# Performance work log

Measured on AMD Instinct MI355X. Metric: run time of the kernel, lower is better.

## Reference

```python
import jax, jax.numpy as jnp
import numpy as np

L = 4        # initial_layers (layers actually run in forward)
DIM = 128    # model dim
NB = 8       # num_blocks per layer
K = 2        # max_active blocks per layer
B = 131072   # batch
FIN = 32     # input features (nn.Linear(32, dim))
PRIORITY = 0.5  # fresh block: success_rate*0.6 + excitement*0.4 = 0.5


def setup_inputs() -> dict:
    key = jax.random.key(0)
    ks = jax.random.split(key, 10)
    s = 0.02
    return {
        "x": jax.random.normal(ks[0], (B, FIN), dtype=jnp.float32),
        "proj_w": jax.random.normal(ks[1], (FIN, DIM)) * s,
        "proj_b": jnp.zeros((DIM,)),
        "pos": jax.random.normal(ks[2], (1, 16, DIM)) * 0.02,
        "sel_w": jax.random.normal(ks[3], (L, DIM, NB)) * s,   # per-layer selector
        "sel_b": jnp.zeros((L, NB)),
        "ln_s": jnp.ones((L, NB, DIM)),                         # per-block LayerNorm
        "ln_b": jnp.zeros((L, NB, DIM)),
        "w1": jax.random.normal(ks[4], (L, NB, DIM, 2 * DIM)) * s,
        "b1": jnp.zeros((L, NB, 2 * DIM)),
        "w2": jax.random.normal(ks[5], (L, NB, 2 * DIM, DIM)) * s,
        "b2": jnp.zeros((L, NB, DIM)),
        "gate": jax.random.normal(ks[6], (L, NB, DIM)) * 0.01,  # torsion_gate
        "cls_w": jax.random.normal(ks[7], (DIM, 2)) * s,
        "cls_b": jnp.zeros((2,)),
        "torsion_field": jnp.zeros((1, DIM)),                   # registered buffer (zeros)
    }


def _block(h, ln_s, ln_b, w1, b1, w2, b2, gate, tf):
    # h: [B, 1, DIM]. LayerNorm(eps=1e-5) -> Linear -> GELU -> Linear -> torsion gate -> 0.5 residual
    mu = h.mean(axis=-1, keepdims=True)
    var = ((h - mu) ** 2).mean(axis=-1, keepdims=True)
    hn = (h - mu) / jnp.sqrt(var + 1e-5) * ln_s + ln_b
    z = jax.nn.gelu(hn @ w1 + b1, approximate=False) @ w2 + b2
    te = jax.nn.sigmoid(gate) * tf           # [1, DIM]
    z = z * (1.0 + te[:, None, :])           # broadcast over seq dim (unsqueeze(1))
    return h + 0.5 * z


def reference(x, proj_w, proj_b, pos, sel_w, sel_b, ln_s, ln_b,
              w1, b1, w2, b2, gate, cls_w, cls_b, torsion_field):
    # input projection + positional slice; seq_len == 1
    h = (x @ proj_w + proj_b)[:, None, :] + pos[:, :1, :]   # [B, 1, DIM]
    for l in range(L):
        scores = jax.nn.sigmoid(h.mean(axis=1) @ sel_w[l] + sel_b[l])  # [B, NB]
        # adjusted[0, i] = scores[0, i]*0.6 + priority*0.4 ; top-k taken on row 0
        adj = scores[0] * 0.6 + PRIORITY * 0.4
        _, top = jax.lax.top_k(adj, K)
        for k in range(K):
            i = top[k]
            h = _block(h, ln_s[l][i], ln_b[l][i], w1[l][i], b1[l][i],
                       w2[l][i], b2[l][i], gate[l][i], torsion_field)
    logits = h.mean(axis=1) @ cls_w + cls_b   # [B, 2]
    return logits, h
```

## Files before the change

### kernel.cpp

```cpp
#include <hip/hip_runtime.h>


typedef __attribute__((ext_vector_type(8))) short s16x8;
typedef __attribute__((ext_vector_type(4))) float f32x4;
typedef __attribute__((ext_vector_type(2))) unsigned u32x2;
typedef unsigned short ushort_t;

#define BATCH 131072
#define TBROWS 32
#define HSTR 132
#define FGSTR 544
#define FQSTR 136

#define WS_IDX 0
#define WS_PRM 64
#define WS_PB  12352
#define WS_PW  12864
#define WS_W1  21056
#define WS_W2  545344
#define WS_DMP 1069632

__device__ inline ushort_t f2bf(float f) {
  unsigned u = __float_as_uint(f);
  u += 0x7fffu + ((u >> 16) & 1u);
  return (ushort_t)(u >> 16);
}
__device__ inline ushort_t f2bf1(float f) {
  return (ushort_t)((__float_as_uint(f) + 0x8000u) >> 16);
}
__device__ inline unsigned f2bf2(float lo, float hi) {
  unsigned a = __float_as_uint(lo) + 0x8000u;
  unsigned b = __float_as_uint(hi) + 0x8000u;
  return __builtin_amdgcn_perm(b, a, 0x07060302u);
}

__device__ inline float dpp_xor1(float v) {
  return __int_as_float(__builtin_amdgcn_update_dpp(
      0, __float_as_int(v), 0xB1 , 0xF, 0xF, true));
}
__device__ inline float dpp_xor2(float v) {
  return __int_as_float(__builtin_amdgcn_update_dpp(
      0, __float_as_int(v), 0x4E , 0xF, 0xF, true));
}

__device__ inline float geluf(float v) {
  float e = __builtin_amdgcn_exp2f(-2.4554670f * v);
  return v * __builtin_amdgcn_rcpf(1.0f + e);
}

__global__ __launch_bounds__(256) void uv6_warm(
    const float* __restrict__ w1, const float* __restrict__ w2,
    float* __restrict__ dump) {
  int gid = blockIdx.x * 256 + threadIdx.x;
  const float4* a = (const float4*)w1;
  const float4* b = (const float4*)w2;
  float s = 0.0f;
#pragma unroll
  for (int i = 0; i < 2; ++i) {
    float4 v = a[gid + i * 131072];
    float4 u = b[gid + i * 131072];
    s += v.x + v.y + v.z + v.w + u.x + u.y + u.z + u.w;
  }
  if (s > 1e30f) dump[0] = s;
}

__global__ __launch_bounds__(1024) void uv6_select(
    const float* __restrict__ x, const float* __restrict__ proj_w,
    const float* __restrict__ proj_b, const float* __restrict__ pos,
    const float* __restrict__ sel_w, const float* __restrict__ sel_b,
    const float* __restrict__ ln_s, const float* __restrict__ ln_b,
    const float* __restrict__ w1, const float* __restrict__ b1,
    const float* __restrict__ w2, const float* __restrict__ b2,
    const float* __restrict__ gate, const float* __restrict__ tf,
    int* __restrict__ wsI) {
  __shared__ float h0[128], hn[128], z1[256];
  __shared__ float red[1024];
  __shared__ float wred[128];
  __shared__ float adjs[8];
  __shared__ int top[2];
  __shared__ float stat[2];
  const int t = threadIdx.x;
  const int lane = t & 63, wv = t >> 6;
  const int n1 = t & 255, dp1 = t >> 8;
  const int n2 = t & 127, dp2 = t >> 7;

  if (t < 128) {
    float a = proj_b[t] + pos[t];
#pragma unroll
    for (int f = 0; f < 32; ++f) a += x[f] * proj_w[f * 128 + t];
    h0[t] = a;
  }
  __syncthreads();

  for (int l = 0; l < 4; ++l) {
    {
      float pp = h0[t >> 3] * sel_w[(l * 128 + (t >> 3)) * 8 + (t & 7)];
      pp += __shfl_xor(pp, 8);
      pp += __shfl_xor(pp, 16);
      pp += __shfl_xor(pp, 32);
      if (lane < 8) wred[wv * 8 + lane] = pp;
    }
    __syncthreads();
    if (t < 8) {
      float sc = sel_b[l * 8 + t];
#pragma unroll
      for (int v = 0; v < 16; ++v) sc += wred[v * 8 + t];
      sc = 1.0f / (1.0f + __expf(-sc));
      adjs[t] = sc * 0.6f + 0.2f;
    }
    __syncthreads();
    if (t == 0) {
      int i0 = 0; float v0 = adjs[0];
      for (int j = 1; j < 8; ++j) if (adjs[j] > v0) { v0 = adjs[j]; i0 = j; }
      int i1 = -1; float v1 = -1e30f;
      for (int j = 0; j < 8; ++j) if (j != i0 && adjs[j] > v1) { v1 = adjs[j]; i1 = j; }
      top[0] = i0; top[1] = i1;
      wsI[2 * l] = i0; wsI[2 * l + 1] = i1;
    }
    __syncthreads();
    for (int kk = 0; kk < 2; ++kk) {
      const int base = l * 8 + top[kk];
      float w1v[32], w2v[32];
      const float* w1p = w1 + (base * 128 + dp1 * 32) * 256 + n1;
      const float* w2p = w2 + (base * 256 + dp2 * 32) * 128 + n2;
#pragma unroll
      for (int j = 0; j < 32; ++j) w1v[j] = w1p[j * 256];
#pragma unroll
      for (int j = 0; j < 32; ++j) w2v[j] = w2p[j * 128];
      if (t < 64) {
        float a = h0[t], b = h0[t + 64];
        float s2 = a + b, q2 = a * a + b * b;
        s2 += __shfl_xor(s2, 1);  q2 += __shfl_xor(q2, 1);
        s2 += __shfl_xor(s2, 2);  q2 += __shfl_xor(q2, 2);
        s2 += __shfl_xor(s2, 4);  q2 += __shfl_xor(q2, 4);
        s2 += __shfl_xor(s2, 8);  q2 += __shfl_xor(q2, 8);
        s2 += __shfl_xor(s2, 16); q2 += __shfl_xor(q2, 16);
        s2 += __shfl_xor(s2, 32); q2 += __shfl_xor(q2, 32);
        if (t == 0) {
          float mu = s2 * (1.0f / 128.0f);
          stat[0] = mu;
          stat[1] = rsqrtf(q2 * (1.0f / 128.0f) - mu * mu + 1e-5f);
        }
      }
      __syncthreads();
      if (t < 128)
        hn[t] = (h0[t] - stat[0]) * stat[1] * ln_s[base * 128 + t] + ln_b[base * 128 + t];
      __syncthreads();
      {
        float a = 0.0f;
#pragma unroll
        for (int j = 0; j < 32; ++j) a += hn[dp1 * 32 + j] * w1v[j];
        red[dp1 * 256 + n1] = a;
      }
      __syncthreads();
      if (t < 256) {
        float z = red[t] + red[256 + t] + red[512 + t] + red[768 + t] + b1[base * 256 + t];
        z1[t] = z * 0.5f * (1.0f + erff(z * 0.70710678118f));
      }
      __syncthreads();
      {
        float a = 0.0f;
#pragma unroll
        for (int j = 0; j < 32; ++j) a += z1[dp2 * 32 + j] * w2v[j];
        red[dp2 * 128 + n2] = a;
      }
      __syncthreads();
      if (t < 128) {
        float z2 = b2[base * 128 + t];
#pragma unroll
        for (int v = 0; v < 8; ++v) z2 += red[v * 128 + t];
        float te = tf[t] * (1.0f / (1.0f + __expf(-gate[base * 128 + t])));
        h0[t] += 0.5f * z2 * (1.0f + te);
      }
      __syncthreads();
    }
  }
}

__global__ __launch_bounds__(256) void uv6_pack(
    const float* __restrict__ w1, const float* __restrict__ w2,
    const float* __restrict__ ln_s, const float* __restrict__ ln_b,
    const float* __restrict__ b1, const float* __restrict__ b2,
    const float* __restrict__ gate, const float* __restrict__ tf,
    const float* __restrict__ proj_w, const float* __restrict__ proj_b,
    const float* __restrict__ pos, const int* __restrict__ wsI,
    ushort_t* __restrict__ w1P, ushort_t* __restrict__ w2P,
    float* __restrict__ wsP, ushort_t* __restrict__ pwP,
    float* __restrict__ pb) {
  const int bx = blockIdx.x;
  const int t = threadIdx.x;
  if (bx < 16) {
    __shared__ ushort_t tile[32768];
    int s = bx >> 1;
    int base = (s >> 1) * 8 + wsI[s];
    if ((bx & 1) == 0) {
      const float* W = w1 + base * 32768;
      const float* LS = ln_s + base * 128;
      int kk = t >> 6, n4 = (t & 63) * 4;
#pragma unroll
      for (int it = 0; it < 16; ++it) {
        int k = it * 8 + kk * 2;
        float4 v0 = *(const float4*)(W + k * 256 + n4);
        float4 v1 = *(const float4*)(W + (k + 1) * 256 + n4);
        float s0 = LS[k], s1 = LS[k + 1];
        int pk = (k >> 5) * 512 + ((k >> 3) & 3) * 128 + (k & 7);
        const float* e0 = (const float*)&v0;
        const float* e1 = (const float*)&v1;
#pragma unroll
        for (int i = 0; i < 4; ++i) {
          int n = n4 + i;
          int pos_ = (n >> 4) * 2048 + pk + (n & 15) * 8;
          *(unsigned*)&tile[pos_] =
              (unsigned)f2bf(e0[i] * s0) | ((unsigned)f2bf(e1[i] * s1) << 16);
        }
      }
      __syncthreads();
      ushort_t* dst = w1P + s * 32768;
#pragma unroll
      for (int it = 0; it < 16; ++it)
        *(uint4*)(dst + (it * 256 + t) * 8) = *(const uint4*)(tile + (it * 256 + t) * 8);
    } else {
      const float* W = w2 + base * 32768;
      int kk = t >> 5, n4 = (t & 31) * 4;
      float te4[4];
#pragma unroll
      for (int i = 0; i < 4; ++i)
        te4[i] = 0.5f * (1.0f + tf[n4 + i] *
                 (1.0f / (1.0f + __expf(-gate[base * 128 + n4 + i]))));
#pragma unroll
      for (int it = 0; it < 16; ++it) {
        int k = it * 16 + kk * 2;
        float4 v0 = *(const float4*)(W + k * 128 + n4);
        float4 v1 = *(const float4*)(W + (k + 1) * 128 + n4);
        int pk = (k >> 5) * 512 + ((k >> 3) & 3) * 128 + (k & 7);
        const float* e0 = (const float*)&v0;
        const float* e1 = (const float*)&v1;
#pragma unroll
        for (int i = 0; i < 4; ++i) {
          int n = n4 + i;
          int pos_ = (n >> 4) * 4096 + pk + (n & 15) * 8;
          *(unsigned*)&tile[pos_] =
              (unsigned)f2bf(e0[i] * te4[i]) | ((unsigned)f2bf(e1[i] * te4[i]) << 16);
        }
      }
      __syncthreads();
      ushort_t* dst = w2P + s * 32768;
#pragma unroll
      for (int it = 0; it < 16; ++it)
        *(uint4*)(dst + (it * 256 + t) * 8) = *(const uint4*)(tile + (it * 256 + t) * 8);
    }
    return;
  }
  if (bx < 24) {
    int s = bx - 16, n = t;
    int base = (s >> 1) * 8 + wsI[s];
    float a = b1[base * 256 + n];
#pragma unroll 16
    for (int k = 0; k < 128; ++k)
      a += ln_b[base * 128 + k] * w1[(base * 128 + k) * 256 + n];
    wsP[s * 384 + n] = a;
    if (n < 128) {
      float te = tf[n] * (1.0f / (1.0f + __expf(-gate[base * 128 + n])));
      wsP[s * 384 + 256 + n] = 0.5f * (1.0f + te) * b2[base * 128 + n];
    }
    return;
  }
  int gid = (bx - 24) * 256 + t;
  if (gid < 4096) {
    int j = gid & 7, ln = (gid >> 3) & 63, nt = gid >> 9;
    int k = (ln >> 4) * 8 + j, n = nt * 16 + (ln & 15);
    pwP[gid] = f2bf(proj_w[k * 128 + n]);
  } else if (gid < 4224) {
    int d = gid - 4096;
    pb[d] = proj_b[d] + pos[d];
  }
}

__global__ __launch_bounds__(256, 4) void uv6_main(
    const float* __restrict__ x, const float* __restrict__ cls_w,
    const float* __restrict__ cls_b, const float* __restrict__ wsP,
    const float* __restrict__ pb, const ushort_t* __restrict__ pwP,
    const ushort_t* __restrict__ w1P, const ushort_t* __restrict__ w2P,
    float* __restrict__ out) {
  __shared__ float hbuf[TBROWS * HSTR];
  __shared__ ushort_t frag[16 * FGSTR];

  const int tid = threadIdx.x;
  const int w = tid >> 6, lane = tid & 63, q = lane >> 4, m0 = lane & 15;
  const int r = tid >> 3, p = tid & 7;
  const int rt_r = r >> 4, m_r = r & 15;
  const long rowbase = (long)blockIdx.x * TBROWS;
  ushort_t* fb = &frag[q * FQSTR + m0 * 8];

  {
    float4 xv = *(const float4*)(x + (rowbase + r) * 32 + p * 4);
    unsigned u01 = f2bf2(xv.x, xv.y), u23 = f2bf2(xv.z, xv.w);
    ushort_t* dst = &frag[(rt_r * 8) * FGSTR + (p >> 1) * FQSTR + m_r * 8 + (p & 1) * 4];
    *(unsigned*)dst = u01;
    *(unsigned*)(dst + 2) = u23;
  }
  __syncthreads();

  {
    s16x8 bp0 = *(const s16x8*)(pwP + ((2 * w + 0) * 64 + lane) * 8);
    s16x8 bp1 = *(const s16x8*)(pwP + ((2 * w + 1) * 64 + lane) * 8);
    float bv0 = pb[(2 * w + 0) * 16 + m0];
    float bv1 = pb[(2 * w + 1) * 16 + m0];
    f32x4 acc[2][2];
#pragma unroll
    for (int rt = 0; rt < 2; ++rt) {
      acc[rt][0] = (f32x4){bv0, bv0, bv0, bv0};
      acc[rt][1] = (f32x4){bv1, bv1, bv1, bv1};
    }
#pragma unroll
    for (int rt = 0; rt < 2; ++rt) {
      s16x8 af = *(const s16x8*)&fb[(rt * 8) * FGSTR];
      acc[rt][0] = __builtin_amdgcn_mfma_f32_16x16x32_bf16(af, bp0, acc[rt][0], 0, 0, 0);
      acc[rt][1] = __builtin_amdgcn_mfma_f32_16x16x32_bf16(af, bp1, acc[rt][1], 0, 0, 0);
    }
#pragma unroll
    for (int rt = 0; rt < 2; ++rt)
#pragma unroll
      for (int ni = 0; ni < 2; ++ni) {
        int col = (2 * w + ni) * 16 + m0;
#pragma unroll
        for (int reg = 0; reg < 4; ++reg)
          hbuf[(rt * 16 + 4 * q + reg) * HSTR + col] = acc[rt][ni][reg];
      }
  }
  __syncthreads();

  float* outH = out + (size_t)BATCH * 2;

  for (int s = 0; s < 8; ++s) {
    const float* c1 = wsP + s * 384;
    const float* c2 = c1 + 256;
    const ushort_t* w1s = w1P + s * 32768;
    const ushort_t* w2s = w2P + s * 32768;

    s16x8 bfr1[4][4];
#pragma unroll
    for (int ni = 0; ni < 4; ++ni)
#pragma unroll
      for (int ks = 0; ks < 4; ++ks)
        bfr1[ni][ks] = *(const s16x8*)(w1s + (((4 * w + ni) * 4 + ks) * 64 + lane) * 8);

    {
      const float* hr = hbuf + r * HSTR + p * 16;
      float hv[16];
#pragma unroll
      for (int i = 0; i < 4; ++i)
        *(float4*)(hv + i * 4) = *(const float4*)(hr + i * 4);
      float sum = 0.0f, ssq = 0.0f;
#pragma unroll
      for (int i = 0; i < 16; ++i) { sum += hv[i]; ssq += hv[i] * hv[i]; }
      sum += dpp_xor1(sum); ssq += dpp_xor1(ssq);
      sum += dpp_xor2(sum); ssq += dpp_xor2(ssq);
      sum += __shfl_xor(sum, 4); ssq += __shfl_xor(ssq, 4);
      float mu = sum * (1.0f / 128.0f);
      float rstd = rsqrtf(ssq * (1.0f / 128.0f) - mu * mu + 1e-5f);
      float nmu = -mu * rstd;
#pragma unroll
      for (int g = 0; g < 2; ++g) {
        union { unsigned u[4]; s16x8 v; } tv;
#pragma unroll
        for (int jj = 0; jj < 4; ++jj) {
          float a = fmaf(hv[g * 8 + jj * 2], rstd, nmu);
          float b = fmaf(hv[g * 8 + jj * 2 + 1], rstd, nmu);
          tv.u[jj] = f2bf2(a, b);
        }
        int kb = p >> 1, kq = (p & 1) * 2 + g;
        *(s16x8*)&frag[(rt_r * 8 + kb) * FGSTR + kq * FQSTR + m_r * 8] = tv.v;
      }
    }
    __syncthreads();

    f32x4 a1[2][4];
#pragma unroll
    for (int ni = 0; ni < 4; ++ni) {
      f32x4 bv = *(const f32x4*)&c1[(4 * w + ni) * 16 + 4 * q];
#pragma unroll
      for (int rt = 0; rt < 2; ++rt) a1[rt][ni] = bv;
    }
#pragma unroll
    for (int ks = 0; ks < 4; ++ks) {
      s16x8 hf[2];
#pragma unroll
      for (int rt = 0; rt < 2; ++rt)
        hf[rt] = *(const s16x8*)&fb[(rt * 8 + ks) * FGSTR];
#pragma unroll
      for (int rt = 0; rt < 2; ++rt)
#pragma unroll
        for (int ni = 0; ni < 4; ++ni)
          a1[rt][ni] = __builtin_amdgcn_mfma_f32_16x16x32_bf16(bfr1[ni][ks], hf[rt], a1[rt][ni], 0, 0, 0);
    }
    __syncthreads();

    s16x8 bfr2[2][8];
#pragma unroll
    for (int ni = 0; ni < 2; ++ni)
#pragma unroll
      for (int ks = 0; ks < 8; ++ks)
        bfr2[ni][ks] = *(const s16x8*)(w2s + (((2 * w + ni) * 8 + ks) * 64 + lane) * 8);
    float cv0 = c2[(2 * w + 0) * 16 + m0];
    float cv1 = c2[(2 * w + 1) * 16 + m0];

    {
      int j0 = 4 * (q & 1), kqb = q >> 1;
#pragma unroll
      for (int ni = 0; ni < 4; ++ni) {
        int kb = 2 * w + (ni >> 1);
        int kq = (2 * ni + kqb) & 3;
#pragma unroll
        for (int rt = 0; rt < 2; ++rt) {
          unsigned lo = f2bf2(geluf(a1[rt][ni][0]), geluf(a1[rt][ni][1]));
          unsigned hi = f2bf2(geluf(a1[rt][ni][2]), geluf(a1[rt][ni][3]));
          *(u32x2*)&frag[(rt * 8 + kb) * FGSTR + kq * FQSTR + m0 * 8 + j0] =
              (u32x2){lo, hi};
        }
      }
    }
    __syncthreads();

    f32x4 a2[2][2];
#pragma unroll
    for (int rt = 0; rt < 2; ++rt) {
      a2[rt][0] = (f32x4){cv0, cv0, cv0, cv0};
      a2[rt][1] = (f32x4){cv1, cv1, cv1, cv1};
    }
#pragma unroll
    for (int kb = 0; kb < 8; ++kb) {
      s16x8 af[2];
#pragma unroll
      for (int rt = 0; rt < 2; ++rt)
        af[rt] = *(const s16x8*)&fb[(rt * 8 + kb) * FGSTR];
#pragma unroll
      for (int rt = 0; rt < 2; ++rt) {
        a2[rt][0] = __builtin_amdgcn_mfma_f32_16x16x32_bf16(af[rt], bfr2[0][kb], a2[rt][0], 0, 0, 0);
        a2[rt][1] = __builtin_amdgcn_mfma_f32_16x16x32_bf16(af[rt], bfr2[1][kb], a2[rt][1], 0, 0, 0);
      }
    }

#pragma unroll
    for (int rt = 0; rt < 2; ++rt)
#pragma unroll
      for (int ni = 0; ni < 2; ++ni) {
        int col = (2 * w + ni) * 16 + m0;
#pragma unroll
        for (int reg = 0; reg < 4; ++reg)
          hbuf[(rt * 16 + 4 * q + reg) * HSTR + col] += a2[rt][ni][reg];
      }
    __syncthreads();
  }

#pragma unroll
  for (int it = 0; it < 4; ++it) {
    int p4 = it * 256 + tid;
    int row = p4 >> 5, c = (p4 & 31) * 4;
    float4 o = *(const float4*)(hbuf + row * HSTR + c);
    *(float4*)(outH + rowbase * 128 + p4 * 4) = o;
  }

  {
    const float* hr = hbuf + r * HSTR + p * 16;
    float l0 = 0.0f, l1 = 0.0f;
#pragma unroll
    for (int i = 0; i < 16; i += 4) {
      float4 v = *(const float4*)(hr + i);
      int c = (p * 16 + i) * 2;
      l0 += v.x * cls_w[c] + v.y * cls_w[c + 2] + v.z * cls_w[c + 4] + v.w * cls_w[c + 6];
      l1 += v.x * cls_w[c + 1] + v.y * cls_w[c + 3] + v.z * cls_w[c + 5] + v.w * cls_w[c + 7];
    }
    l0 += dpp_xor1(l0); l1 += dpp_xor1(l1);
    l0 += dpp_xor2(l0); l1 += dpp_xor2(l1);
    l0 += __shfl_xor(l0, 4); l1 += __shfl_xor(l1, 4);
    if (p == 0) {
      float2 lg = {l0 + cls_b[0], l1 + cls_b[1]};
      *(float2*)(out + (rowbase + r) * 2) = lg;
    }
  }
}

extern "C" void kernel_launch(void* const* d_in, const int* in_sizes, int n_in,
                              void* d_out, int out_size, void* d_ws, size_t ws_size,
                              hipStream_t stream) {
  (void)in_sizes; (void)n_in; (void)out_size; (void)ws_size;
  const float* x      = (const float*)d_in[0];
  const float* proj_w = (const float*)d_in[1];
  const float* proj_b = (const float*)d_in[2];
  const float* pos    = (const float*)d_in[3];
  const float* sel_w  = (const float*)d_in[4];
  const float* sel_b  = (const float*)d_in[5];
  const float* ln_s   = (const float*)d_in[6];
  const float* ln_b   = (const float*)d_in[7];
  const float* w1     = (const float*)d_in[8];
  const float* b1     = (const float*)d_in[9];
  const float* w2     = (const float*)d_in[10];
  const float* b2     = (const float*)d_in[11];
  const float* gate   = (const float*)d_in[12];
  const float* cls_w  = (const float*)d_in[13];
  const float* cls_b  = (const float*)d_in[14];
  const float* tf     = (const float*)d_in[15];

  char* ws = (char*)d_ws;
  int* wsI        = (int*)(ws + WS_IDX);
  float* wsP      = (float*)(ws + WS_PRM);
  float* pb       = (float*)(ws + WS_PB);
  ushort_t* pwP   = (ushort_t*)(ws + WS_PW);
  ushort_t* w1P   = (ushort_t*)(ws + WS_W1);
  ushort_t* w2P   = (ushort_t*)(ws + WS_W2);
  float* dump     = (float*)(ws + WS_DMP);
  float* outF     = (float*)d_out;

  uv6_warm<<<512, 256, 0, stream>>>(w1, w2, dump);
  uv6_select<<<1, 1024, 0, stream>>>(x, proj_w, proj_b, pos, sel_w, sel_b, ln_s,
                                     ln_b, w1, b1, w2, b2, gate, tf, wsI);
  uv6_pack<<<41, 256, 0, stream>>>(w1, w2, ln_s, ln_b, b1, b2, gate, tf,
                                   proj_w, proj_b, pos, wsI, w1P, w2P, wsP,
                                   pwP, pb);
  uv6_main<<<BATCH / TBROWS, 256, 0, stream>>>(x, cls_w, cls_b, wsP, pb, pwP,
                                               w1P, w2P, outF);
}
```

Baseline: 362.8 us.

## Rewrite select kernel as single-wave shuffle version; lighter barriers and MFMA priority

The single-block routing kernel moves from 1024 threads with many LDS reductions and __syncthreads to a single 64-lane wave. That wave keeps h in registers and uses shuffles for all reductions and matvecs, which removes barrier latency on this serial critical path but leaves much less parallelism for the weight streaming. The main kernel swaps __syncthreads for an lgkmcnt wait plus raw s_barrier with a sched_barrier, and raises wave priority around the MFMA loops. An unused helper is removed.

```diff
diff --git a/kernel.cpp b/kernel.cpp
--- a/kernel.cpp
+++ b/kernel.cpp
@@ -20,13 +20,16 @@
 #define WS_W2  545344
 #define WS_DMP 1069632
 
+#define BARRIER_LDS() do {                                   \
+    asm volatile("s_waitcnt lgkmcnt(0)" ::: "memory");       \
+    __builtin_amdgcn_s_barrier();                            \
+    __builtin_amdgcn_sched_barrier(0);                       \
+  } while (0)
+
 __device__ inline ushort_t f2bf(float f) {
   unsigned u = __float_as_uint(f);
   u += 0x7fffu + ((u >> 16) & 1u);
   return (ushort_t)(u >> 16);
-}
-__device__ inline ushort_t f2bf1(float f) {
-  return (ushort_t)((__float_as_uint(f) + 0x8000u) >> 16);
 }
 __device__ inline unsigned f2bf2(float lo, float hi) {
   unsigned a = __float_as_uint(lo) + 0x8000u;
@@ -64,7 +67,7 @@
   if (s > 1e30f) dump[0] = s;
 }
 
-__global__ __launch_bounds__(1024) void uv6_select(
+__global__ __launch_bounds__(64) void uv6_select(
     const float* __restrict__ x, const float* __restrict__ proj_w,
     const float* __restrict__ proj_b, const float* __restrict__ pos,
     const float* __restrict__ sel_w, const float* __restrict__ sel_b,
@@ -73,106 +76,102 @@
     const float* __restrict__ w2, const float* __restrict__ b2,
     const float* __restrict__ gate, const float* __restrict__ tf,
     int* __restrict__ wsI) {
-  __shared__ float h0[128], hn[128], z1[256];
-  __shared__ float red[1024];
-  __shared__ float wred[128];
-  __shared__ float adjs[8];
-  __shared__ int top[2];
-  __shared__ float stat[2];
-  const int t = threadIdx.x;
-  const int lane = t & 63, wv = t >> 6;
-  const int n1 = t & 255, dp1 = t >> 8;
-  const int n2 = t & 127, dp2 = t >> 7;
-
-  if (t < 128) {
-    float a = proj_b[t] + pos[t];
-#pragma unroll
-    for (int f = 0; f < 32; ++f) a += x[f] * proj_w[f * 128 + t];
-    h0[t] = a;
-  }
-  __syncthreads();
+  const int lane = threadIdx.x;
+
+  float xv = x[lane & 31];
+  float ha = proj_b[lane] + pos[lane];
+  float hb = proj_b[lane + 64] + pos[lane + 64];
+#pragma unroll
+  for (int f = 0; f < 32; ++f) {
+    float xf = __shfl(xv, f);
+    ha = fmaf(xf, proj_w[f * 128 + lane], ha);
+    hb = fmaf(xf, proj_w[f * 128 + lane + 64], hb);
+  }
 
   for (int l = 0; l < 4; ++l) {
-    {
-      float pp = h0[t >> 3] * sel_w[(l * 128 + (t >> 3)) * 8 + (t & 7)];
-      pp += __shfl_xor(pp, 8);
-      pp += __shfl_xor(pp, 16);
-      pp += __shfl_xor(pp, 32);
-      if (lane < 8) wred[wv * 8 + lane] = pp;
-    }
-    __syncthreads();
-    if (t < 8) {
-      float sc = sel_b[l * 8 + t];
-#pragma unroll
-      for (int v = 0; v < 16; ++v) sc += wred[v * 8 + t];
-      sc = 1.0f / (1.0f + __expf(-sc));
-      adjs[t] = sc * 0.6f + 0.2f;
-    }
-    __syncthreads();
-    if (t == 0) {
-      int i0 = 0; float v0 = adjs[0];
-      for (int j = 1; j < 8; ++j) if (adjs[j] > v0) { v0 = adjs[j]; i0 = j; }
-      int i1 = -1; float v1 = -1e30f;
-      for (int j = 0; j < 8; ++j) if (j != i0 && adjs[j] > v1) { v1 = adjs[j]; i1 = j; }
-      top[0] = i0; top[1] = i1;
-      wsI[2 * l] = i0; wsI[2 * l + 1] = i1;
-    }
-    __syncthreads();
+    float sc[8];
+#pragma unroll
+    for (int n = 0; n < 8; ++n) {
+      sc[n] = fmaf(ha, sel_w[(l * 128 + lane) * 8 + n],
+                   hb * sel_w[(l * 128 + lane + 64) * 8 + n]);
+    }
+#pragma unroll
+    for (int n = 0; n < 8; ++n) {
+      sc[n] += __shfl_xor(sc[n], 1);
+      sc[n] += __shfl_xor(sc[n], 2);
+      sc[n] += __shfl_xor(sc[n], 4);
+      sc[n] += __shfl_xor(sc[n], 8);
+      sc[n] += __shfl_xor(sc[n], 16);
+      sc[n] += __shfl_xor(sc[n], 32);
+    }
+    float adj[8];
+#pragma unroll
+    for (int n = 0; n < 8; ++n) {
+      float s = 1.0f / (1.0f + __expf(-(sc[n] + sel_b[l * 8 + n])));
+      adj[n] = s * 0.6f + 0.2f;
+    }
+    int i0 = 0; float v0 = adj[0];
+#pragma unroll
+    for (int j = 1; j < 8; ++j) if (adj[j] > v0) { v0 = adj[j]; i0 = j; }
+    int i1 = -1; float v1 = -1e30f;
+#pragma unroll
+    for (int j = 0; j < 8; ++j) if (j != i0 && adj[j] > v1) { v1 = adj[j]; i1 = j; }
+    if (lane == 0) { wsI[2 * l] = i0; wsI[2 * l + 1] = i1; }
+
+#pragma unroll 1
     for (int kk = 0; kk < 2; ++kk) {
-      const int base = l * 8 + top[kk];
-      float w1v[32], w2v[32];
-      const float* w1p = w1 + (base * 128 + dp1 * 32) * 256 + n1;
-      const float* w2p = w2 + (base * 256 + dp2 * 32) * 128 + n2;
-#pragma unroll
-      for (int j = 0; j < 32; ++j) w1v[j] = w1p[j * 256];
-#pragma unroll
-      for (int j = 0; j < 32; ++j) w2v[j] = w2p[j * 128];
-      if (t < 64) {
-        float a = h0[t], b = h0[t + 64];
-        float s2 = a + b, q2 = a * a + b * b;
-        s2 += __shfl_xor(s2, 1);  q2 += __shfl_xor(q2, 1);
-        s2 += __shfl_xor(s2, 2);  q2 += __shfl_xor(q2, 2);
-        s2 += __shfl_xor(s2, 4);  q2 += __shfl_xor(q2, 4);
-        s2 += __shfl_xor(s2, 8);  q2 += __shfl_xor(q2, 8);
-        s2 += __shfl_xor(s2, 16); q2 += __shfl_xor(q2, 16);
-        s2 += __shfl_xor(s2, 32); q2 += __shfl_xor(q2, 32);
-        if (t == 0) {
-          float mu = s2 * (1.0f / 128.0f);
-          stat[0] = mu;
-          stat[1] = rsqrtf(q2 * (1.0f / 128.0f) - mu * mu + 1e-5f);
+      const int base = l * 8 + (kk == 0 ? i0 : i1);
+      float s2 = ha + hb, q2 = ha * ha + hb * hb;
+      s2 += __shfl_xor(s2, 1);  q2 += __shfl_xor(q2, 1);
+      s2 += __shfl_xor(s2, 2);  q2 += __shfl_xor(q2, 2);
+      s2 += __shfl_xor(s2, 4);  q2 += __shfl_xor(q2, 4);
+      s2 += __shfl_xor(s2, 8);  q2 += __shfl_xor(q2, 8);
+      s2 += __shfl_xor(s2, 16); q2 += __shfl_xor(q2, 16);
+      s2 += __shfl_xor(s2, 32); q2 += __shfl_xor(q2, 32);
+      float mu = s2 * (1.0f / 128.0f);
+      float rstd = rsqrtf(q2 * (1.0f / 128.0f) - mu * mu + 1e-5f);
+      float na = (ha - mu) * rstd * ln_s[base * 128 + lane] + ln_b[base * 128 + lane];
+      float nb = (hb - mu) * rstd * ln_s[base * 128 + lane + 64] + ln_b[base * 128 + lane + 64];
+
+      float z[4];
+#pragma unroll
+      for (int jj = 0; jj < 4; ++jj) z[jj] = b1[base * 256 + 64 * jj + lane];
+      const float* W1 = w1 + base * 32768;
+#pragma unroll 8
+      for (int d = 0; d < 64; ++d) {
+        float u = __shfl(na, d);
+#pragma unroll
+        for (int jj = 0; jj < 4; ++jj)
+          z[jj] = fmaf(u, W1[d * 256 + 64 * jj + lane], z[jj]);
+      }
+#pragma unroll 8
+      for (int d = 0; d < 64; ++d) {
+        float u = __shfl(nb, d);
+#pragma unroll
+        for (int jj = 0; jj < 4; ++jj)
+          z[jj] = fmaf(u, W1[(64 + d) * 256 + 64 * jj + lane], z[jj]);
+      }
+#pragma unroll
+      for (int jj = 0; jj < 4; ++jj)
+        z[jj] = z[jj] * 0.5f * (1.0f + erff(z[jj] * 0.70710678118f));
+
+      float s0 = 0.0f, s1 = 0.0f;
+      const float* W2 = w2 + base * 32768;
+#pragma unroll
+      for (int jj = 0; jj < 4; ++jj) {
+#pragma unroll 8
+        for (int k = 0; k < 64; ++k) {
+          float u = __shfl(z[jj], k);
+          s0 = fmaf(u, W2[(jj * 64 + k) * 128 + lane], s0);
+          s1 = fmaf(u, W2[(jj * 64 + k) * 128 + lane + 64], s1);
         }
       }
-      __syncthreads();
-      if (t < 128)
-        hn[t] = (h0[t] - stat[0]) * stat[1] * ln_s[base * 128 + t] + ln_b[base * 128 + t];
-      __syncthreads();
-      {
-        float a = 0.0f;
-#pragma unroll
-        for (int j = 0; j < 32; ++j) a += hn[dp1 * 32 + j] * w1v[j];
-        red[dp1 * 256 + n1] = a;
-      }
-      __syncthreads();
-      if (t < 256) {
-        float z = red[t] + red[256 + t] + red[512 + t] + red[768 + t] + b1[base * 256 + t];
-        z1[t] = z * 0.5f * (1.0f + erff(z * 0.70710678118f));
-      }
-      __syncthreads();
-      {
-        float a = 0.0f;
-#pragma unroll
-        for (int j = 0; j < 32; ++j) a += z1[dp2 * 32 + j] * w2v[j];
-        red[dp2 * 128 + n2] = a;
-      }
-      __syncthreads();
-      if (t < 128) {
-        float z2 = b2[base * 128 + t];
-#pragma unroll
-        for (int v = 0; v < 8; ++v) z2 += red[v * 128 + t];
-        float te = tf[t] * (1.0f / (1.0f + __expf(-gate[base * 128 + t])));
-        h0[t] += 0.5f * z2 * (1.0f + te);
-      }
-      __syncthreads();
+      s0 += b2[base * 128 + lane];
+      s1 += b2[base * 128 + lane + 64];
+      float te0 = tf[lane] * (1.0f / (1.0f + __expf(-gate[base * 128 + lane])));
+      float te1 = tf[lane + 64] * (1.0f / (1.0f + __expf(-gate[base * 128 + lane + 64])));
+      ha += 0.5f * s0 * (1.0f + te0);
+      hb += 0.5f * s1 * (1.0f + te1);
     }
   }
 }
@@ -373,7 +372,7 @@
         *(s16x8*)&frag[(rt_r * 8 + kb) * FGSTR + kq * FQSTR + m_r * 8] = tv.v;
       }
     }
-    __syncthreads();
+    BARRIER_LDS();
 
     f32x4 a1[2][4];
 #pragma unroll
@@ -382,6 +381,7 @@
 #pragma unroll
       for (int rt = 0; rt < 2; ++rt) a1[rt][ni] = bv;
     }
+    __builtin_amdgcn_s_setprio(1);
 #pragma unroll
     for (int ks = 0; ks < 4; ++ks) {
       s16x8 hf[2];
@@ -394,7 +394,8 @@
         for (int ni = 0; ni < 4; ++ni)
           a1[rt][ni] = __builtin_amdgcn_mfma_f32_16x16x32_bf16(bfr1[ni][ks], hf[rt], a1[rt][ni], 0, 0, 0);
     }
-    __syncthreads();
+    __builtin_amdgcn_s_setprio(0);
+    BARRIER_LDS();
 
     s16x8 bfr2[2][8];
 #pragma unroll
@@ -420,7 +421,7 @@
         }
       }
     }
-    __syncthreads();
+    BARRIER_LDS();
 
     f32x4 a2[2][2];
 #pragma unroll
@@ -428,6 +429,7 @@
       a2[rt][0] = (f32x4){cv0, cv0, cv0, cv0};
       a2[rt][1] = (f32x4){cv1, cv1, cv1, cv1};
     }
+    __builtin_amdgcn_s_setprio(1);
 #pragma unroll
     for (int kb = 0; kb < 8; ++kb) {
       s16x8 af[2];
@@ -440,6 +442,7 @@
         a2[rt][1] = __builtin_amdgcn_mfma_f32_16x16x32_bf16(af[rt], bfr2[1][kb], a2[rt][1], 0, 0, 0);
       }
     }
+    __builtin_amdgcn_s_setprio(0);
 
 #pragma unroll
     for (int rt = 0; rt < 2; ++rt)
@@ -450,7 +453,7 @@
         for (int reg = 0; reg < 4; ++reg)
           hbuf[(rt * 16 + 4 * q + reg) * HSTR + col] += a2[rt][ni][reg];
       }
-    __syncthreads();
+    BARRIER_LDS();
   }
 
 #pragma unroll
@@ -513,8 +516,8 @@
   float* outF     = (float*)d_out;
 
   uv6_warm<<<512, 256, 0, stream>>>(w1, w2, dump);
-  uv6_select<<<1, 1024, 0, stream>>>(x, proj_w, proj_b, pos, sel_w, sel_b, ln_s,
-                                     ln_b, w1, b1, w2, b2, gate, tf, wsI);
+  uv6_select<<<1, 64, 0, stream>>>(x, proj_w, proj_b, pos, sel_w, sel_b, ln_s,
+                                   ln_b, w1, b1, w2, b2, gate, tf, wsI);
   uv6_pack<<<41, 256, 0, stream>>>(w1, w2, ln_s, ln_b, b1, b2, gate, tf,
                                    proj_w, proj_b, pos, wsI, w1P, w2P, wsP,
                                    pwP, pb);
```

Measured after the change: 452.7 us. 24.8% more time.
